# Optimization experiments

Hardware: AMD Instinct MI355X
Metric: run time of the kernel (lower is better)

The kernel has to match this reference:

```python
import jax, jax.numpy as jnp
import numpy as np

HID, H, KV, D = 2048, 16, 4, 128
ROPE_THETA = 10000.0
GATE_NORM = 16.0


def _rope_cos_sin(n, d, dtype=jnp.float32):
    inv_freq = 1.0 / (ROPE_THETA ** (jnp.arange(0, d, 2, dtype=jnp.float32) / d))
    freqs = jnp.arange(n, dtype=jnp.float32)[:, None] * inv_freq[None, :]  # (n, d/2)
    cos = jnp.cos(freqs).astype(dtype)[None, :, None, :]  # (1, n, 1, d/2)
    sin = jnp.sin(freqs).astype(dtype)[None, :, None, :]
    return cos, sin


def _apply_rotary(x, cos, sin):
    # x: (b, n, h, d); rotate-half (NeoX) convention over full head dim
    x1, x2 = jnp.split(x, 2, axis=-1)
    return jnp.concatenate([x1 * cos - x2 * sin, x2 * cos + x1 * sin], axis=-1)


def setup_inputs() -> dict:
    key = jax.random.key(0)
    k1, k2, k3, k4, k5 = jax.random.split(key, 5)
    s = 0.02  # realistic init scale for weights
    return {
        "hidden_states": jax.random.normal(k1, (1, 2048, HID), dtype=jnp.float32),
        "Wq": jax.random.normal(k2, (HID, H * D), dtype=jnp.float32) * s,
        "Wk": jax.random.normal(k3, (HID, KV * D), dtype=jnp.float32) * s,
        "Wv": jax.random.normal(k4, (HID, KV * D), dtype=jnp.float32) * s,
        "Wo": jax.random.normal(k5, (H * D, HID), dtype=jnp.float32) * s,
    }


def _forward(hidden_states, Wq, Wk, Wv, Wo):
    b, n, _ = hidden_states.shape
    groups = H // KV

    q = hidden_states @ Wq            # (b, n, H*D)
    k = hidden_states @ Wk            # (b, n, KV*D)
    v = hidden_states @ Wv            # (b, n, KV*D)
    # pool_g: AdaptiveAvgPool1d(KV*D) on a length-(KV*D) last dim == identity
    g = k

    q = q.reshape(b, n, H, D)
    k = k.reshape(b, n, KV, D)
    v = v.reshape(b, n, KV, D)
    g = g.reshape(b, n, KV, D)

    # GQA repeat to H heads
    k = jnp.repeat(k, groups, axis=2)
    v = jnp.repeat(v, groups, axis=2)
    g = jnp.repeat(g, groups, axis=2)

    sq, sk, sv = q, k, v  # raw (pre-softmax) tensors for the attention branch

    # GLA branch inputs: softmax'd q/k, log-sigmoid gates
    qs = jax.nn.softmax(q.astype(jnp.float32), axis=-1)
    ks = jax.nn.softmax(k.astype(jnp.float32), axis=-1)
    gl = jax.nn.log_sigmoid(g.astype(jnp.float32)) / GATE_NORM

    # rotary on raw q/k (seqlen_offset = 0)
    cos, sin = _rope_cos_sin(n, D)
    sq = _apply_rotary(sq, cos, sin)
    sk = _apply_rotary(sk, cos, sin)

    # --- gated linear attention recurrence (chunk_gla math, scale=1) ---
    def step(S, inp):
        q_t, k_t, v_t, g_t = inp  # each (b, H, D)
        S = S * jnp.exp(g_t)[..., None] + k_t[..., None] * v_t[..., None, :]
        o_t = jnp.einsum('bhk,bhkv->bhv', q_t, S)
        return S, o_t

    xs = tuple(jnp.moveaxis(a, 1, 0) for a in (qs, ks, v, gl))  # (n, b, H, D)
    S0 = jnp.zeros((b, H, D, D), dtype=jnp.float32)
    _, o_gla = jax.lax.scan(step, S0, xs)
    o_gla = jnp.moveaxis(o_gla, 0, 1)  # (b, n, H, D)

    # --- causal softmax attention (flash_attn_func, full window) ---
    scale = D ** -0.5
    scores = jnp.einsum('bqhd,bkhd->bhqk', sq, sk) * scale
    causal = jnp.tril(jnp.ones((n, n), dtype=bool))
    scores = jnp.where(causal[None, None], scores, jnp.finfo(scores.dtype).min)
    attn = jax.nn.softmax(scores, axis=-1)
    y = jnp.einsum('bhqk,bkhd->bqhd', attn, sv)

    o = 0.5 * y + 0.5 * o_gla
    o = o.reshape(b, n, H * D).astype(hidden_states.dtype)
    return o @ Wo


def reference(hidden_states, Wq, Wk, Wv, Wo):
    return _forward(hidden_states, Wq, Wk, Wv, Wo)
```

## Files before the change

### kernel.cpp

```cpp
#include <hip/hip_runtime.h>
#include <hip/hip_bf16.h>

typedef __bf16 bf16x8 __attribute__((ext_vector_type(8)));
typedef float f32x4 __attribute__((ext_vector_type(4)));
typedef float f32x16 __attribute__((ext_vector_type(16)));
typedef unsigned u32x4 __attribute__((ext_vector_type(4)));

#define MFMA16(a,b,c) __builtin_amdgcn_mfma_f32_16x16x32_bf16((a),(b),(c),0,0,0)
#define MFMA32(a,b,c) __builtin_amdgcn_mfma_f32_32x32x16_bf16((a),(b),(c),0,0,0)

__device__ __forceinline__ float bf2f(const __hip_bfloat16 h){ return __bfloat162float(h); }
__device__ __forceinline__ __hip_bfloat16 f2bf(float f){ return __float2bfloat16(f); }
__device__ __forceinline__ __bf16 f2raw(float f){
  return __builtin_bit_cast(__bf16, __builtin_bit_cast(unsigned short, __float2bfloat16(f)));
}

__device__ __forceinline__ unsigned pk2(float a, float b){
  unsigned lo = __builtin_bit_cast(unsigned short, __float2bfloat16(a));
  unsigned hi = __builtin_bit_cast(unsigned short, __float2bfloat16(b));
  return lo | (hi << 16);
}
__device__ __forceinline__ void pl32swap(unsigned &x, unsigned &y){
  asm volatile("v_permlane32_swap_b32 %0, %1" : "+v"(x), "+v"(y));
}
__device__ __forceinline__ void gload16(const void* g, void* l){
  __builtin_amdgcn_global_load_lds((const __attribute__((address_space(1))) unsigned int*)g,
                                   (__attribute__((address_space(3))) unsigned int*)l, 16, 0, 0);
}

__device__ __forceinline__ size_t pk_idx(int grp, int ntile, int t, int d){
  int t32 = t >> 5, ql = t & 31, i = d >> 4, kh = (d >> 3) & 1, j = d & 7;
  return ((size_t)(grp*ntile + t32)*8 + i)*512 + (kh*32 + ql)*8 + j;
}
__device__ __forceinline__ size_t ep_idx(int grp, int t, int d){
  int t16 = t >> 4, lr = t & 15, f = d >> 5, lg = (d >> 3) & 3, j = d & 7;
  return (((size_t)grp*128 + t16)*4 + f)*512 + (lg*16 + lr)*8 + j;
}

__global__ void k_rope_table(float* __restrict__ ct, float* __restrict__ st){
  int e = blockIdx.x*256 + threadIdx.x;
  if (e >= 2048*64) return;
  int t = e >> 6, d = e & 63;
  float inv = expf(-(float)d * 0.14391156831212787f);
  float ang = (float)t * inv;
  ct[e] = cosf(ang);
  st[e] = sinf(ang);
}

__global__ void k_cvt_bf16(const float* __restrict__ in, __hip_bfloat16* __restrict__ out, int n4){
  int i = blockIdx.x*256 + threadIdx.x;
  if (i >= n4) return;
  float4 v = reinterpret_cast<const float4*>(in)[i];
  ushort4 o;
  o.x = __builtin_bit_cast(unsigned short, f2bf(v.x));
  o.y = __builtin_bit_cast(unsigned short, f2bf(v.y));
  o.z = __builtin_bit_cast(unsigned short, f2bf(v.z));
  o.w = __builtin_bit_cast(unsigned short, f2bf(v.w));
  reinterpret_cast<ushort4*>(out)[i] = o;
}

__global__ __launch_bounds__(256) void k_transpose_w(const float* __restrict__ Wq,
                                                     const float* __restrict__ Wk,
                                                     const float* __restrict__ Wv,
                                                     const float* __restrict__ Wo,
                                                     __hip_bfloat16* __restrict__ WqkvT,
                                                     __hip_bfloat16* __restrict__ WoT){
  __shared__ float tile[64][65];
  int id = blockIdx.x;
  const float* in; __hip_bfloat16* out; int C, bx, by;
  if (id < 1024)      { in=Wq; out=WqkvT;                         C=2048; bx=id&31;          by=id>>5; }
  else if (id < 1280) { int i=id-1024; in=Wk; out=WqkvT+(size_t)2048*2048; C=512; bx=i&7;    by=i>>3; }
  else if (id < 1536) { int i=id-1280; in=Wv; out=WqkvT+(size_t)2560*2048; C=512; bx=i&7;    by=i>>3; }
  else                { int i=id-1536; in=Wo; out=WoT;            C=2048; bx=i&31;           by=i>>5; }
  const int R = 2048;
  int ct_ = bx*64, rt = by*64;
  int tx = threadIdx.x & 63, ty = threadIdx.x >> 6;
  #pragma unroll
  for (int i=0;i<16;++i){ int lr = i*4 + ty; tile[lr][tx] = in[(size_t)(rt+lr)*C + ct_+tx]; }
  __syncthreads();
  #pragma unroll
  for (int i=0;i<16;++i){ int lr = i*4 + ty; out[(size_t)(ct_+lr)*R + rt+tx] = f2bf(tile[tx][lr]); }
}

__global__ __launch_bounds__(128) void k_gemm_lds2(const __hip_bfloat16* __restrict__ A,
                                                   const __hip_bfloat16* __restrict__ BT,
                                                   float* __restrict__ C, int M, int N, int K){
  __shared__ __hip_bfloat16 As[128*64];
  __shared__ __hip_bfloat16 Bs[64*64];
  int nwg = gridDim.x;
  int cpx = nwg >> 3;
  int wg  = blockIdx.x;
  int swz = (wg & 7)*cpx + (wg >> 3);
  int nbx = N >> 6;
  int bn = (swz % nbx)*64, bm = (swz / nbx)*128;
  int tid = threadIdx.x, w = tid >> 6, l = tid & 63, lr = l & 15, lg = l >> 4;
  int wr = w*64;
  int srow = tid >> 3;
  int scol = (tid & 7)*8;
  f32x4 z = {0.f,0.f,0.f,0.f};
  f32x4 acc[4][4];
  #pragma unroll
  for (int i=0;i<4;++i){
    #pragma unroll
    for (int j=0;j<4;++j) acc[i][j] = z;
  }
  for (int bk=0; bk<K; bk+=64){
    #pragma unroll
    for (int i=0;i<8;++i)
      gload16(&A[(size_t)(bm + i*16 + srow)*K + bk + scol], &As[i*1024 + tid*8]);
    #pragma unroll
    for (int i=0;i<4;++i)
      gload16(&BT[(size_t)(bn + i*16 + srow)*K + bk + scol], &Bs[i*1024 + tid*8]);
    __syncthreads();
    __builtin_amdgcn_s_setprio(1);
    #pragma unroll
    for (int kk=0; kk<2; ++kk){
      bf16x8 af[4], bfr[4];
      #pragma unroll
      for (int mi=0;mi<4;++mi) af[mi]  = *reinterpret_cast<const bf16x8*>(&As[(wr+mi*16+lr)*64 + kk*32 + lg*8]);
      #pragma unroll
      for (int ni=0;ni<4;++ni) bfr[ni] = *reinterpret_cast<const bf16x8*>(&Bs[(ni*16+lr)*64 + kk*32 + lg*8]);
      #pragma unroll
      for (int mi=0;mi<4;++mi){
        #pragma unroll
        for (int ni=0;ni<4;++ni)
          acc[mi][ni] = MFMA16(af[mi], bfr[ni], acc[mi][ni]);
      }
    }
    __builtin_amdgcn_s_setprio(0);
    __syncthreads();
  }
  #pragma unroll
  for (int mi=0;mi<4;++mi){
    #pragma unroll
    for (int ni=0;ni<4;++ni){
      #pragma unroll
      for (int r=0;r<4;++r)
        C[(size_t)(bm+wr+mi*16+lg*4+r)*N + (bn+ni*16+lr)] = acc[mi][ni][r];
    }
  }
}

__global__ __launch_bounds__(128) void k_gates(const float* __restrict__ qkv,
                                               float* __restrict__ bt_all,
                                               float* __restrict__ eC){
  int c = blockIdx.x, kv = blockIdx.y, k = threadIdx.x;
  float b = 0.f;
  #pragma unroll 8
  for (int t=0;t<64;++t){
    float x = qkv[(size_t)(c*64+t)*3072 + 2048 + kv*128 + k];
    float gl = (fminf(x,0.f) - log1pf(expf(-fabsf(x)))) * 0.09016844005f;
    b += gl;
    bt_all[(size_t)(c*64+t)*512 + kv*128 + k] = b;
  }
  eC[((size_t)kv*32 + c)*128 + k] = exp2f(b);
}

__global__ __launch_bounds__(256) void k_qkpost(const float* __restrict__ qkv, const float* __restrict__ ct,
                                                const float* __restrict__ st, const float* __restrict__ bt_all,
                                                __hip_bfloat16* __restrict__ qpk, __hip_bfloat16* __restrict__ qep,
                                                __hip_bfloat16* __restrict__ kpk, __hip_bfloat16* __restrict__ ke,
                                                __hip_bfloat16* __restrict__ kep){
  int bid = blockIdx.x;
  int i = threadIdx.x & 63;
  if (bid < 8192){
    int g = bid*4 + (threadIdx.x >> 6);
    int t = g >> 4, h = g & 15;
    size_t base = (size_t)t*3072 + h*128;
    float a = qkv[base + i], b = qkv[base + 64 + i];
    float mx = fmaxf(a,b);
    #pragma unroll
    for (int off=1; off<64; off<<=1) mx = fmaxf(mx, __shfl_xor(mx, off));
    float ea = expf(a-mx), eb = expf(b-mx);
    float sm = ea+eb;
    #pragma unroll
    for (int off=1; off<64; off<<=1) sm += __shfl_xor(sm, off);
    float r = 1.0f/sm;
    const float* bp = &bt_all[(size_t)t*512 + (h>>2)*128];
    qep[ep_idx(h, t, i)]    = f2bf(exp2f(bp[i])    * (ea*r));
    qep[ep_idx(h, t, 64+i)] = f2bf(exp2f(bp[64+i]) * (eb*r));
    const float scale = 0.12751745f;
    float co = ct[t*64+i], si = st[t*64+i];
    qpk[pk_idx(h, 64, t, i)]    = f2bf((a*co - b*si)*scale);
    qpk[pk_idx(h, 64, t, 64+i)] = f2bf((b*co + a*si)*scale);
  } else {
    int g = (bid-8192)*4 + (threadIdx.x >> 6);
    int t = g >> 2, kv = g & 3;
    size_t base = (size_t)t*3072 + 2048 + kv*128;
    float a = qkv[base + i], b = qkv[base + 64 + i];
    float mx = fmaxf(a,b);
    #pragma unroll
    for (int off=1; off<64; off<<=1) mx = fmaxf(mx, __shfl_xor(mx, off));
    float ea = expf(a-mx), eb = expf(b-mx);
    float sm = ea+eb;
    #pragma unroll
    for (int off=1; off<64; off<<=1) sm += __shfl_xor(sm, off);
    float r = 1.0f/sm;
    const float* bp = &bt_all[(size_t)t*512 + kv*128];
    float kea = exp2f(-bp[i])    * (ea*r);
    float keb = exp2f(-bp[64+i]) * (eb*r);
    size_t ob = ((size_t)t*4 + kv)*128;
    ke[ob+i]    = f2bf(kea);
    ke[ob+64+i] = f2bf(keb);
    kep[ep_idx(kv, t, i)]    = f2bf(kea);
    kep[ep_idx(kv, t, 64+i)] = f2bf(keb);
    float co = ct[t*64+i], si = st[t*64+i];
    kpk[pk_idx(kv, 64, t, i)]    = f2bf(a*co - b*si);
    kpk[pk_idx(kv, 64, t, 64+i)] = f2bf(b*co + a*si);
  }
}

__global__ __launch_bounds__(256) void k_vprep(const float* __restrict__ qkv,
                                               __hip_bfloat16* __restrict__ vt,
                                               __hip_bfloat16* __restrict__ vpk,
                                               __hip_bfloat16* __restrict__ vpk16){
  __shared__ float lds[64*132];
  int s = blockIdx.x, kv = blockIdx.y;
  int tid = threadIdx.x;
  #pragma unroll
  for (int it=0; it<8; ++it){
    int i = it*256 + tid;
    int t = i >> 5, dc = (i & 31)*4;
    float4 v = *reinterpret_cast<const float4*>(&qkv[(size_t)(s*64+t)*3072 + 2560 + kv*128 + dc]);
    *reinterpret_cast<float4*>(&lds[t*132 + dc]) = v;
  }
  __syncthreads();
  #pragma unroll
  for (int it=0; it<4; ++it){
    int i = it*256 + tid;
    int d = i >> 3, tg = (i & 7)*8;
    bf16x8 o;
    #pragma unroll
    for (int j=0;j<8;++j) o[j] = f2raw(lds[(tg+j)*132 + d]);
    *reinterpret_cast<bf16x8*>(&vt[((size_t)kv*128 + d)*2048 + s*64 + tg]) = o;
  }
  #pragma unroll
  for (int it=0; it<4; ++it){
    int j2 = it*256 + tid;
    int dt = j2 >> 8, kq = (j2 >> 6) & 3, l = j2 & 63;
    int ts = kq*16 + (l>>5)*8, ds = dt*32 + (l&31);
    bf16x8 o;
    #pragma unroll
    for (int j=0;j<8;++j) o[j] = f2raw(lds[(ts+j)*132 + ds]);
    *reinterpret_cast<bf16x8*>(&vpk[((((size_t)kv*32 + s)*4 + dt)*4 + kq)*512 + l*8]) = o;
  }
  #pragma unroll
  for (int it=0; it<4; ++it){
    int j3 = it*256 + tid;
    int oc = j3 >> 7, f2 = (j3 >> 6) & 1, l = j3 & 63;
    int ts = f2*32 + (l>>4)*8, ds = oc*16 + (l&15);
    bf16x8 o;
    #pragma unroll
    for (int j=0;j<8;++j) o[j] = f2raw(lds[(ts+j)*132 + ds]);
    *reinterpret_cast<bf16x8*>(&vpk16[((((size_t)kv*32 + s)*8 + oc)*2 + f2)*512 + l*8]) = o;
  }
}

__global__ __launch_bounds__(256) void k_ckv(const __hip_bfloat16* __restrict__ ke,
                                             const __hip_bfloat16* __restrict__ vt,
                                             float* __restrict__ ckv){
  __shared__ __hip_bfloat16 kt[128*72];
  int c = blockIdx.x, kv = blockIdx.y;
  int tid = threadIdx.x, w = tid>>6, l = tid&63, lr=l&15, lg=l>>4;
  int wr = (w>>1)*64, wc = (w&1)*64;
  #pragma unroll
  for (int r=0;r<4;++r){
    int idx = r*256 + tid;
    int t  = idx >> 4;
    int k0 = (idx & 15)*8;
    bf16x8 v = *reinterpret_cast<const bf16x8*>(&ke[((size_t)(c*64+t)*4 + kv)*128 + k0]);
    #pragma unroll
    for (int j=0;j<8;++j) kt[(k0+j)*72 + t] = __builtin_bit_cast(__hip_bfloat16, (unsigned short)__builtin_bit_cast(unsigned short, v[j]));
  }
  __syncthreads();
  f32x4 z = {0.f,0.f,0.f,0.f};
  f32x4 acc[4][4];
  #pragma unroll
  for (int i=0;i<4;++i){
    #pragma unroll
    for (int j=0;j<4;++j) acc[i][j]=z;
  }
  size_t sb = (size_t)kv*32 + c;
  #pragma unroll
  for (int kf2=0;kf2<2;++kf2){
    bf16x8 af[4], bfr[4];
    #pragma unroll
    for (int mi=0;mi<4;++mi)
      af[mi] = *reinterpret_cast<const bf16x8*>(&kt[(wr+mi*16+lr)*72 + kf2*32 + lg*8]);
    #pragma unroll
    for (int ni=0;ni<4;++ni)
      bfr[ni] = *reinterpret_cast<const bf16x8*>(&vt[((size_t)kv*128 + wc+ni*16+lr)*2048 + c*64 + kf2*32 + lg*8]);
    #pragma unroll
    for (int mi=0;mi<4;++mi){
      #pragma unroll
      for (int ni=0;ni<4;++ni)
        acc[mi][ni] = MFMA16(af[mi], bfr[ni], acc[mi][ni]);
    }
  }
  #pragma unroll
  for (int mi=0;mi<4;++mi){
    #pragma unroll
    for (int ni=0;ni<4;++ni){
      #pragma unroll
      for (int r=0;r<4;++r)
        ckv[(sb*128 + wr+mi*16+lg*4+r)*128 + wc+ni*16+lr] = acc[mi][ni][r];
    }
  }
}

__global__ __launch_bounds__(256) void k_scan(const float* __restrict__ ckv, const float* __restrict__ eC,
                                              __hip_bfloat16* __restrict__ Stp){
  __shared__ float lds[8*128];
  int kv = blockIdx.y, bx = blockIdx.x;
  int tid = threadIdx.x;
  int kloc = tid >> 5;
  int kd  = bx*8 + kloc;
  int vd  = (tid*4) & 127;
  int oc = tid >> 5, lr = (tid >> 1) & 15, jh = (tid & 1)*4;
  int f  = bx >> 2, lg = bx & 3;
  float s0=0.f,s1=0.f,s2=0.f,s3=0.f;
  size_t sb0 = (size_t)kv*32;
  float e = eC[sb0*128 + kd];
  float4 u = reinterpret_cast<const float4*>(&ckv[(sb0*128 + kd)*128 + vd])[0];
  for (int c=0;c<32;++c){
    size_t sb = sb0 + c;
    float e_n = 0.f; float4 u_n = {0.f,0.f,0.f,0.f};
    if (c < 31){
      e_n = eC[(sb+1)*128 + kd];
      u_n = reinterpret_cast<const float4*>(&ckv[((sb+1)*128 + kd)*128 + vd])[0];
    }
    float4 cur = {s0,s1,s2,s3};
    *reinterpret_cast<float4*>(&lds[kloc*128 + vd]) = cur;
    __syncthreads();
    unsigned w0 = pk2(lds[(jh+0)*128 + oc*16+lr], lds[(jh+1)*128 + oc*16+lr]);
    unsigned w1 = pk2(lds[(jh+2)*128 + oc*16+lr], lds[(jh+3)*128 + oc*16+lr]);
    unsigned* dst = reinterpret_cast<unsigned*>(&Stp[((sb*8+oc)*4+f)*512 + (lg*16+lr)*8 + jh]);
    dst[0]=w0; dst[1]=w1;
    __syncthreads();
    s0 = (s0 + u.x)*e; s1 = (s1 + u.y)*e; s2 = (s2 + u.z)*e; s3 = (s3 + u.w)*e;
    e = e_n; u = u_n;
  }
}

__global__ __launch_bounds__(256) void k_attn(const __hip_bfloat16* __restrict__ qpk,
                                              const __hip_bfloat16* __restrict__ kpk,
                                              const __hip_bfloat16* __restrict__ vpk,
                                              float* __restrict__ ocomb){
  __shared__ __hip_bfloat16 OW[4][32][138];
  __shared__ float mW[4][32], lW[4][32];
  int h = blockIdx.y, kvh = h >> 2;
  int tid = threadIdx.x, w = tid >> 6, l = tid & 63;
  int ql = l & 31, kh = l >> 5;

  #pragma unroll 1
  for (int half=0; half<2; ++half){
    int qt = half ? (63 - (int)blockIdx.x) : (int)blockIdx.x;
    int qbase = qt*32;
    int qg = qbase + ql;

    bf16x8 qf[8];
    #pragma unroll
    for (int i=0;i<8;++i)
      qf[i] = *reinterpret_cast<const bf16x8*>(&qpk[((size_t)(h*64 + qt)*8 + i)*512 + l*8]);

    f32x16 zz = {0.f,0.f,0.f,0.f,0.f,0.f,0.f,0.f,0.f,0.f,0.f,0.f,0.f,0.f,0.f,0.f};
    f32x16 of[4];
    #pragma unroll
    for (int dt=0;dt<4;++dt) of[dt] = zz;
    float m = -1e30f, ll = 0.f;

    int nstep = qt/2 + 1;
    for (int s=w; s<nstep; s+=4){
      int kb = s*64;
      bool last = (s == nstep-1);
      f32x16 s0 = zz, s1 = zz;
      #pragma unroll
      for (int i=0;i<8;++i){
        bf16x8 k0 = *reinterpret_cast<const bf16x8*>(&kpk[((size_t)(kvh*64 + 2*s)*8 + i)*512 + l*8]);
        s0 = MFMA32(k0, qf[i], s0);
      }
      #pragma unroll
      for (int i=0;i<8;++i){
        bf16x8 k1 = *reinterpret_cast<const bf16x8*>(&kpk[((size_t)(kvh*64 + 2*s+1)*8 + i)*512 + l*8]);
        s1 = MFMA32(k1, qf[i], s1);
      }
      if (last){
        #pragma unroll
        for (int r=0;r<16;++r){
          int kr = (r&3) + 8*(r>>2) + 4*kh;
          if (kb + kr > qg)      s0[r] = -1e30f;
          if (kb + 32 + kr > qg) s1[r] = -1e30f;
        }
      }
      float pmax = fmaxf(s0[0], s1[0]);
      #pragma unroll
      for (int r=1;r<16;++r) pmax = fmaxf(pmax, fmaxf(s0[r], s1[r]));
      pmax = fmaxf(pmax, __shfl_xor(pmax, 32));
      if (!__all(pmax <= m + 11.54f)){
        float nm = fmaxf(m, pmax);
        float ef = exp2f(m - nm);
        ll *= ef;
        #pragma unroll
        for (int dt=0;dt<4;++dt){
          #pragma unroll
          for (int r=0;r<16;++r) of[dt][r] *= ef;
        }
        m = nm;
      }
      float ps = 0.f;
      #pragma unroll
      for (int r=0;r<16;++r){ s0[r] = exp2f(s0[r]-m); ps += s0[r]; }
      #pragma unroll
      for (int r=0;r<16;++r){ s1[r] = exp2f(s1[r]-m); ps += s1[r]; }
      ps += __shfl_xor(ps, 32);
      ll += ps;
      unsigned pw[4][4];
      {
        unsigned a,b;
        a = pk2(s0[0],s0[1]);   b = pk2(s0[4],s0[5]);   pl32swap(a,b); pw[0][0]=a; pw[0][2]=b;
        a = pk2(s0[2],s0[3]);   b = pk2(s0[6],s0[7]);   pl32swap(a,b); pw[0][1]=a; pw[0][3]=b;
        a = pk2(s0[8],s0[9]);   b = pk2(s0[12],s0[13]); pl32swap(a,b); pw[1][0]=a; pw[1][2]=b;
        a = pk2(s0[10],s0[11]); b = pk2(s0[14],s0[15]); pl32swap(a,b); pw[1][1]=a; pw[1][3]=b;
        a = pk2(s1[0],s1[1]);   b = pk2(s1[4],s1[5]);   pl32swap(a,b); pw[2][0]=a; pw[2][2]=b;
        a = pk2(s1[2],s1[3]);   b = pk2(s1[6],s1[7]);   pl32swap(a,b); pw[2][1]=a; pw[2][3]=b;
        a = pk2(s1[8],s1[9]);   b = pk2(s1[12],s1[13]); pl32swap(a,b); pw[3][0]=a; pw[3][2]=b;
        a = pk2(s1[10],s1[11]); b = pk2(s1[14],s1[15]); pl32swap(a,b); pw[3][1]=a; pw[3][3]=b;
      }
      #pragma unroll
      for (int dt=0; dt<4; ++dt){
        #pragma unroll
        for (int kq=0; kq<4; ++kq){
          bf16x8 vf = *reinterpret_cast<const bf16x8*>(&vpk[((((size_t)kvh*32 + s)*4 + dt)*4 + kq)*512 + l*8]);
          u32x4 pu = {pw[kq][0], pw[kq][1], pw[kq][2], pw[kq][3]};
          bf16x8 pb = __builtin_bit_cast(bf16x8, pu);
          of[dt] = MFMA32(vf, pb, of[dt]);
        }
      }
    }
    if (kh == 0){ mW[w][ql] = m; lW[w][ql] = ll; }
    #pragma unroll
    for (int dt=0; dt<4; ++dt){
      #pragma unroll
      for (int rp=0; rp<4; ++rp){
        unsigned lo = pk2(of[dt][rp*4+0], of[dt][rp*4+1]);
        unsigned hi = pk2(of[dt][rp*4+2], of[dt][rp*4+3]);
        unsigned* dst = reinterpret_cast<unsigned*>(&OW[w][ql][dt*32 + 8*rp + 4*kh]);
        dst[0] = lo; dst[1] = hi;
      }
    }
    __syncthreads();
    int q = tid >> 3, db = (tid & 7)*16;
    float m0=mW[0][q], m1=mW[1][q], m2=mW[2][q], m3=mW[3][q];
    float ms = fmaxf(fmaxf(m0,m1), fmaxf(m2,m3));
    float fac[4] = {exp2f(m0-ms), exp2f(m1-ms), exp2f(m2-ms), exp2f(m3-ms)};
    float lt = fac[0]*lW[0][q] + fac[1]*lW[1][q] + fac[2]*lW[2][q] + fac[3]*lW[3][q];
    float acc[16];
    #pragma unroll
    for (int j=0;j<16;++j) acc[j] = 0.f;
    #pragma unroll
    for (int wv=0; wv<4; ++wv){
      const unsigned* src = reinterpret_cast<const unsigned*>(&OW[wv][q][db]);
      float fx = fac[wv];
      #pragma unroll
      for (int j=0;j<8;++j){
        unsigned u = src[j];
        acc[2*j]   += fx * __builtin_bit_cast(float, u << 16);
        acc[2*j+1] += fx * __builtin_bit_cast(float, u & 0xffff0000u);
      }
    }
    float inv = 0.5f / lt;
    float4 o0 = {acc[0]*inv, acc[1]*inv, acc[2]*inv, acc[3]*inv};
    float4 o1 = {acc[4]*inv, acc[5]*inv, acc[6]*inv, acc[7]*inv};
    float4 o2 = {acc[8]*inv, acc[9]*inv, acc[10]*inv, acc[11]*inv};
    float4 o3 = {acc[12]*inv, acc[13]*inv, acc[14]*inv, acc[15]*inv};
    float4* dst = reinterpret_cast<float4*>(&ocomb[(size_t)(qbase+q)*2048 + h*128 + db]);
    dst[0]=o0; dst[1]=o1; dst[2]=o2; dst[3]=o3;
    __syncthreads();
  }
}

__global__ __launch_bounds__(256) void k_gla_out(const __hip_bfloat16* __restrict__ qep,
                                                 const __hip_bfloat16* __restrict__ kep,
                                                 const __hip_bfloat16* __restrict__ vpk16,
                                                 const __hip_bfloat16* __restrict__ Stp,
                                                 const float* __restrict__ ocomb,
                                                 __hip_bfloat16* __restrict__ obf){
  __shared__ __hip_bfloat16 ldsp[4*16*72];
  int c = blockIdx.x, h = blockIdx.y, kvh = h >> 2;
  int tid = threadIdx.x, w = tid>>6, l = tid&63, lr = l&15, lg = l>>4;
  int t0 = c*64, r0 = w*16;
  __hip_bfloat16* myp = &ldsp[w*16*72];
  bf16x8 qef[4];
  #pragma unroll
  for (int f=0; f<4; ++f)
    qef[f] = *reinterpret_cast<const bf16x8*>(&qep[(((size_t)h*128 + c*4 + w)*4 + f)*512 + l*8]);
  f32x4 z = {0.f,0.f,0.f,0.f};
  f32x4 of[8];
  #pragma unroll
  for (int oc=0;oc<8;++oc) of[oc]=z;
  __builtin_amdgcn_s_setprio(1);
  #pragma unroll
  for (int oc=0; oc<8; ++oc){
    #pragma unroll
    for (int f=0; f<4; ++f){
      bf16x8 sfr = *reinterpret_cast<const bf16x8*>(&Stp[((((size_t)kvh*32 + c)*8 + oc)*4 + f)*512 + l*8]);
      of[oc] = MFMA16(qef[f], sfr, of[oc]);
    }
  }
  f32x4 sacc[4] = {z,z,z,z};
  #pragma unroll
  for (int cb=0; cb<4; ++cb){
    #pragma unroll
    for (int f=0; f<4; ++f){
      bf16x8 kf = *reinterpret_cast<const bf16x8*>(&kep[(((size_t)kvh*128 + c*4 + cb)*4 + f)*512 + l*8]);
      sacc[cb] = MFMA16(qef[f], kf, sacc[cb]);
    }
  }
  __builtin_amdgcn_s_setprio(0);
  #pragma unroll
  for (int cb=0; cb<4; ++cb){
    #pragma unroll
    for (int r=0;r<4;++r){
      int s_ = cb*16 + lr;
      int t_ = r0 + lg*4 + r;
      float v = (s_ <= t_) ? sacc[cb][r] : 0.f;
      myp[(lg*4 + r)*72 + cb*16 + lr] = f2bf(v);
    }
  }
  bf16x8 pf[2];
  #pragma unroll
  for (int kf2=0;kf2<2;++kf2)
    pf[kf2] = *reinterpret_cast<const bf16x8*>(&myp[lr*72 + kf2*32 + lg*8]);
  __builtin_amdgcn_s_setprio(1);
  #pragma unroll
  for (int oc=0; oc<8; ++oc){
    #pragma unroll
    for (int kf2=0;kf2<2;++kf2){
      bf16x8 vf = *reinterpret_cast<const bf16x8*>(&vpk16[((((size_t)kvh*32 + c)*8 + oc)*2 + kf2)*512 + l*8]);
      of[oc] = MFMA16(pf[kf2], vf, of[oc]);
    }
  }
  __builtin_amdgcn_s_setprio(0);
  #pragma unroll
  for (int oc=0;oc<8;++oc){
    #pragma unroll
    for (int r=0;r<4;++r){
      int row = t0 + r0 + lg*4 + r;
      int col = h*128 + oc*16 + lr;
      float prev = ocomb[(size_t)row*2048 + col];
      obf[(size_t)row*2048 + col] = f2bf(prev + 0.5f*of[oc][r]);
    }
  }
}

extern "C" void kernel_launch(void* const* d_in, const int* in_sizes, int n_in,
                              void* d_out, int out_size, void* d_ws, size_t ws_size,
                              hipStream_t stream) {
  const float* hs = (const float*)d_in[0];
  const float* Wq = (const float*)d_in[1];
  const float* Wk = (const float*)d_in[2];
  const float* Wv = (const float*)d_in[3];
  const float* Wo = (const float*)d_in[4];
  float* out = (float*)d_out;

  char* base = (char*)d_ws;
  size_t off = 0;
  auto alloc = [&](size_t bytes) -> void* {
    void* p = base + off;
    off = (off + bytes + 255) & ~(size_t)255;
    return p;
  };

  float*          ropeC  = (float*)alloc(2048*64*4);
  float*          ropeS  = (float*)alloc(2048*64*4);
  __hip_bfloat16* hsb    = (__hip_bfloat16*)alloc((size_t)4194304*2);
  __hip_bfloat16* WqkvT  = (__hip_bfloat16*)alloc((size_t)3072*2048*2);
  __hip_bfloat16* WoT    = (__hip_bfloat16*)alloc((size_t)4194304*2);
  float*          qkv    = (float*)alloc((size_t)2048*3072*4);
  __hip_bfloat16* qpk    = (__hip_bfloat16*)alloc((size_t)4194304*2);
  __hip_bfloat16* kpk    = (__hip_bfloat16*)alloc((size_t)1048576*2);
  __hip_bfloat16* vt     = (__hip_bfloat16*)alloc((size_t)1048576*2);
  __hip_bfloat16* vpk    = (__hip_bfloat16*)alloc((size_t)1048576*2);
  __hip_bfloat16* vpk16  = (__hip_bfloat16*)alloc((size_t)1048576*2);
  __hip_bfloat16* qep    = (__hip_bfloat16*)alloc((size_t)4194304*2);
  __hip_bfloat16* ke     = (__hip_bfloat16*)alloc((size_t)1048576*2);
  __hip_bfloat16* kep    = (__hip_bfloat16*)alloc((size_t)1048576*2);
  float*          bt_all = (float*)alloc((size_t)1048576*4);
  float*          eC     = (float*)alloc((size_t)4*32*128*4);
  float*          ckv    = (float*)alloc((size_t)4*32*128*128*4);
  __hip_bfloat16* Stp    = (__hip_bfloat16*)alloc((size_t)4*32*128*128*2);
  float*          ocomb  = qkv;
  __hip_bfloat16* obf    = hsb;

  if (off > ws_size) return;

  k_rope_table<<<512, 256, 0, stream>>>(ropeC, ropeS);
  k_cvt_bf16<<<4096, 256, 0, stream>>>(hs, hsb, 1048576);
  k_transpose_w<<<dim3(2560), 256, 0, stream>>>(Wq, Wk, Wv, Wo, WqkvT, WoT);

  k_gemm_lds2<<<dim3(768), 128, 0, stream>>>(hsb, WqkvT, qkv, 2048, 3072, 2048);

  k_gates<<<dim3(32,4), 128, 0, stream>>>(qkv, bt_all, eC);
  k_qkpost<<<dim3(10240), 256, 0, stream>>>(qkv, ropeC, ropeS, bt_all, qpk, qep, kpk, ke, kep);
  k_vprep<<<dim3(32,4), 256, 0, stream>>>(qkv, vt, vpk, vpk16);

  k_ckv<<<dim3(32,4), 256, 0, stream>>>(ke, vt, ckv);
  k_scan<<<dim3(16,4), 256, 0, stream>>>(ckv, eC, Stp);

  k_attn<<<dim3(32,16), 256, 0, stream>>>(qpk, kpk, vpk, ocomb);
  k_gla_out<<<dim3(32,16), 256, 0, stream>>>(qep, kep, vpk16, Stp, ocomb, obf);

  k_gemm_lds2<<<dim3(512), 128, 0, stream>>>(obf, WoT, out, 2048, 2048, 2048);
}
```

Baseline: 268.0 us.

## Split attention blocks to one query tile each and halve LDS merge buffer

```diff
diff --git a/kernel.cpp b/kernel.cpp
--- a/kernel.cpp
+++ b/kernel.cpp
@@ -346,136 +346,168 @@
                                               const __hip_bfloat16* __restrict__ kpk,
                                               const __hip_bfloat16* __restrict__ vpk,
                                               float* __restrict__ ocomb){
-  __shared__ __hip_bfloat16 OW[4][32][138];
+  __shared__ __hip_bfloat16 OW[4][32][70];
   __shared__ float mW[4][32], lW[4][32];
   int h = blockIdx.y, kvh = h >> 2;
   int tid = threadIdx.x, w = tid >> 6, l = tid & 63;
   int ql = l & 31, kh = l >> 5;
-
-  #pragma unroll 1
-  for (int half=0; half<2; ++half){
-    int qt = half ? (63 - (int)blockIdx.x) : (int)blockIdx.x;
-    int qbase = qt*32;
-    int qg = qbase + ql;
-
-    bf16x8 qf[8];
-    #pragma unroll
-    for (int i=0;i<8;++i)
-      qf[i] = *reinterpret_cast<const bf16x8*>(&qpk[((size_t)(h*64 + qt)*8 + i)*512 + l*8]);
-
-    f32x16 zz = {0.f,0.f,0.f,0.f,0.f,0.f,0.f,0.f,0.f,0.f,0.f,0.f,0.f,0.f,0.f,0.f};
-    f32x16 of[4];
-    #pragma unroll
-    for (int dt=0;dt<4;++dt) of[dt] = zz;
-    float m = -1e30f, ll = 0.f;
-
-    int nstep = qt/2 + 1;
-    for (int s=w; s<nstep; s+=4){
-      int kb = s*64;
-      bool last = (s == nstep-1);
-      f32x16 s0 = zz, s1 = zz;
-      #pragma unroll
-      for (int i=0;i<8;++i){
-        bf16x8 k0 = *reinterpret_cast<const bf16x8*>(&kpk[((size_t)(kvh*64 + 2*s)*8 + i)*512 + l*8]);
-        s0 = MFMA32(k0, qf[i], s0);
+  int qt = 63 - (int)blockIdx.x;
+  int qbase = qt*32;
+  int qg = qbase + ql;
+
+  bf16x8 qf[8];
+  #pragma unroll
+  for (int i=0;i<8;++i)
+    qf[i] = *reinterpret_cast<const bf16x8*>(&qpk[((size_t)(h*64 + qt)*8 + i)*512 + l*8]);
+
+  f32x16 zz = {0.f,0.f,0.f,0.f,0.f,0.f,0.f,0.f,0.f,0.f,0.f,0.f,0.f,0.f,0.f,0.f};
+  f32x16 of[4];
+  #pragma unroll
+  for (int dt=0;dt<4;++dt) of[dt] = zz;
+  float m = -1e30f, ll = 0.f;
+
+  int nstep = qt/2 + 1;
+  for (int s=w; s<nstep; s+=4){
+    int kb = s*64;
+    bool last = (s == nstep-1);
+    f32x16 s0 = zz, s1 = zz;
+    #pragma unroll
+    for (int i=0;i<8;++i){
+      bf16x8 k0 = *reinterpret_cast<const bf16x8*>(&kpk[((size_t)(kvh*64 + 2*s)*8 + i)*512 + l*8]);
+      s0 = MFMA32(k0, qf[i], s0);
+    }
+    #pragma unroll
+    for (int i=0;i<8;++i){
+      bf16x8 k1 = *reinterpret_cast<const bf16x8*>(&kpk[((size_t)(kvh*64 + 2*s+1)*8 + i)*512 + l*8]);
+      s1 = MFMA32(k1, qf[i], s1);
+    }
+    if (last){
+      #pragma unroll
+      for (int r=0;r<16;++r){
+        int kr = (r&3) + 8*(r>>2) + 4*kh;
+        if (kb + kr > qg)      s0[r] = -1e30f;
+        if (kb + 32 + kr > qg) s1[r] = -1e30f;
       }
-      #pragma unroll
-      for (int i=0;i<8;++i){
-        bf16x8 k1 = *reinterpret_cast<const bf16x8*>(&kpk[((size_t)(kvh*64 + 2*s+1)*8 + i)*512 + l*8]);
-        s1 = MFMA32(k1, qf[i], s1);
+    }
+    float pmax = fmaxf(s0[0], s1[0]);
+    #pragma unroll
+    for (int r=1;r<16;++r) pmax = fmaxf(pmax, fmaxf(s0[r], s1[r]));
+    pmax = fmaxf(pmax, __shfl_xor(pmax, 32));
+    if (!__all(pmax <= m + 11.54f)){
+      float nm = fmaxf(m, pmax);
+      float ef = exp2f(m - nm);
+      ll *= ef;
+      #pragma unroll
+      for (int dt=0;dt<4;++dt){
+        #pragma unroll
+        for (int r=0;r<16;++r) of[dt][r] *= ef;
       }
-      if (last){
-        #pragma unroll
-        for (int r=0;r<16;++r){
-          int kr = (r&3) + 8*(r>>2) + 4*kh;
-          if (kb + kr > qg)      s0[r] = -1e30f;
-          if (kb + 32 + kr > qg) s1[r] = -1e30f;
-        }
+      m = nm;
+    }
+    float ps = 0.f;
+    #pragma unroll
+    for (int r=0;r<16;++r){ s0[r] = exp2f(s0[r]-m); ps += s0[r]; }
+    #pragma unroll
+    for (int r=0;r<16;++r){ s1[r] = exp2f(s1[r]-m); ps += s1[r]; }
+    ps += __shfl_xor(ps, 32);
+    ll += ps;
+    unsigned pw[4][4];
+    {
+      unsigned a,b;
+      a = pk2(s0[0],s0[1]);   b = pk2(s0[4],s0[5]);   pl32swap(a,b); pw[0][0]=a; pw[0][2]=b;
+      a = pk2(s0[2],s0[3]);   b = pk2(s0[6],s0[7]);   pl32swap(a,b); pw[0][1]=a; pw[0][3]=b;
+      a = pk2(s0[8],s0[9]);   b = pk2(s0[12],s0[13]); pl32swap(a,b); pw[1][0]=a; pw[1][2]=b;
+      a = pk2(s0[10],s0[11]); b = pk2(s0[14],s0[15]); pl32swap(a,b); pw[1][1]=a; pw[1][3]=b;
+      a = pk2(s1[0],s1[1]);   b = pk2(s1[4],s1[5]);   pl32swap(a,b); pw[2][0]=a; pw[2][2]=b;
+      a = pk2(s1[2],s1[3]);   b = pk2(s1[6],s1[7]);   pl32swap(a,b); pw[2][1]=a; pw[2][3]=b;
+      a = pk2(s1[8],s1[9]);   b = pk2(s1[12],s1[13]); pl32swap(a,b); pw[3][0]=a; pw[3][2]=b;
+      a = pk2(s1[10],s1[11]); b = pk2(s1[14],s1[15]); pl32swap(a,b); pw[3][1]=a; pw[3][3]=b;
+    }
+    #pragma unroll
+    for (int dt=0; dt<4; ++dt){
+      #pragma unroll
+      for (int kq=0; kq<4; ++kq){
+        bf16x8 vf = *reinterpret_cast<const bf16x8*>(&vpk[((((size_t)kvh*32 + s)*4 + dt)*4 + kq)*512 + l*8]);
+        u32x4 pu = {pw[kq][0], pw[kq][1], pw[kq][2], pw[kq][3]};
+        bf16x8 pb = __builtin_bit_cast(bf16x8, pu);
+        of[dt] = MFMA32(vf, pb, of[dt]);
       }
-      float pmax = fmaxf(s0[0], s1[0]);
-      #pragma unroll
-      for (int r=1;r<16;++r) pmax = fmaxf(pmax, fmaxf(s0[r], s1[r]));
-      pmax = fmaxf(pmax, __shfl_xor(pmax, 32));
-      if (!__all(pmax <= m + 11.54f)){
-        float nm = fmaxf(m, pmax);
-        float ef = exp2f(m - nm);
-        ll *= ef;
-        #pragma unroll
-        for (int dt=0;dt<4;++dt){
-          #pragma unroll
-          for (int r=0;r<16;++r) of[dt][r] *= ef;
-        }
-        m = nm;
-      }
-      float ps = 0.f;
-      #pragma unroll
-      for (int r=0;r<16;++r){ s0[r] = exp2f(s0[r]-m); ps += s0[r]; }
-      #pragma unroll
-      for (int r=0;r<16;++r){ s1[r] = exp2f(s1[r]-m); ps += s1[r]; }
-      ps += __shfl_xor(ps, 32);
-      ll += ps;
-      unsigned pw[4][4];
-      {
-        unsigned a,b;
-        a = pk2(s0[0],s0[1]);   b = pk2(s0[4],s0[5]);   pl32swap(a,b); pw[0][0]=a; pw[0][2]=b;
-        a = pk2(s0[2],s0[3]);   b = pk2(s0[6],s0[7]);   pl32swap(a,b); pw[0][1]=a; pw[0][3]=b;
-        a = pk2(s0[8],s0[9]);   b = pk2(s0[12],s0[13]); pl32swap(a,b); pw[1][0]=a; pw[1][2]=b;
-        a = pk2(s0[10],s0[11]); b = pk2(s0[14],s0[15]); pl32swap(a,b); pw[1][1]=a; pw[1][3]=b;
-        a = pk2(s1[0],s1[1]);   b = pk2(s1[4],s1[5]);   pl32swap(a,b); pw[2][0]=a; pw[2][2]=b;
-        a = pk2(s1[2],s1[3]);   b = pk2(s1[6],s1[7]);   pl32swap(a,b); pw[2][1]=a; pw[2][3]=b;
-        a = pk2(s1[8],s1[9]);   b = pk2(s1[12],s1[13]); pl32swap(a,b); pw[3][0]=a; pw[3][2]=b;
-        a = pk2(s1[10],s1[11]); b = pk2(s1[14],s1[15]); pl32swap(a,b); pw[3][1]=a; pw[3][3]=b;
-      }
-      #pragma unroll
-      for (int dt=0; dt<4; ++dt){
-        #pragma unroll
-        for (int kq=0; kq<4; ++kq){
-          bf16x8 vf = *reinterpret_cast<const bf16x8*>(&vpk[((((size_t)kvh*32 + s)*4 + dt)*4 + kq)*512 + l*8]);
-          u32x4 pu = {pw[kq][0], pw[kq][1], pw[kq][2], pw[kq][3]};
-          bf16x8 pb = __builtin_bit_cast(bf16x8, pu);
-          of[dt] = MFMA32(vf, pb, of[dt]);
-        }
-      }
-    }
-    if (kh == 0){ mW[w][ql] = m; lW[w][ql] = ll; }
-    #pragma unroll
-    for (int dt=0; dt<4; ++dt){
-      #pragma unroll
-      for (int rp=0; rp<4; ++rp){
-        unsigned lo = pk2(of[dt][rp*4+0], of[dt][rp*4+1]);
-        unsigned hi = pk2(of[dt][rp*4+2], of[dt][rp*4+3]);
-        unsigned* dst = reinterpret_cast<unsigned*>(&OW[w][ql][dt*32 + 8*rp + 4*kh]);
-        dst[0] = lo; dst[1] = hi;
-      }
-    }
-    __syncthreads();
-    int q = tid >> 3, db = (tid & 7)*16;
+    }
+  }
+  if (kh == 0){ mW[w][ql] = m; lW[w][ql] = ll; }
+  int q = tid >> 3, db8 = (tid & 7)*8;
+  float fac0, fac1, fac2, fac3, lt;
+  #pragma unroll
+  for (int dt=0; dt<2; ++dt){
+    #pragma unroll
+    for (int rp=0; rp<4; ++rp){
+      unsigned lo = pk2(of[dt][rp*4+0], of[dt][rp*4+1]);
+      unsigned hi = pk2(of[dt][rp*4+2], of[dt][rp*4+3]);
+      unsigned* dst = reinterpret_cast<unsigned*>(&OW[w][ql][dt*32 + 8*rp + 4*kh]);
+      dst[0] = lo; dst[1] = hi;
+    }
+  }
+  __syncthreads();
+  {
     float m0=mW[0][q], m1=mW[1][q], m2=mW[2][q], m3=mW[3][q];
     float ms = fmaxf(fmaxf(m0,m1), fmaxf(m2,m3));
-    float fac[4] = {exp2f(m0-ms), exp2f(m1-ms), exp2f(m2-ms), exp2f(m3-ms)};
-    float lt = fac[0]*lW[0][q] + fac[1]*lW[1][q] + fac[2]*lW[2][q] + fac[3]*lW[3][q];
-    float acc[16];
-    #pragma unroll
-    for (int j=0;j<16;++j) acc[j] = 0.f;
+    fac0=exp2f(m0-ms); fac1=exp2f(m1-ms); fac2=exp2f(m2-ms); fac3=exp2f(m3-ms);
+    lt = fac0*lW[0][q] + fac1*lW[1][q] + fac2*lW[2][q] + fac3*lW[3][q];
+  }
+  float inv = 0.5f / lt;
+  {
+    float acc[8];
+    #pragma unroll
+    for (int j=0;j<8;++j) acc[j] = 0.f;
+    float facv[4] = {fac0, fac1, fac2, fac3};
     #pragma unroll
     for (int wv=0; wv<4; ++wv){
-      const unsigned* src = reinterpret_cast<const unsigned*>(&OW[wv][q][db]);
-      float fx = fac[wv];
-      #pragma unroll
-      for (int j=0;j<8;++j){
+      const unsigned* src = reinterpret_cast<const unsigned*>(&OW[wv][q][db8]);
+      float fx = facv[wv];
+      #pragma unroll
+      for (int j=0;j<4;++j){
         unsigned u = src[j];
         acc[2*j]   += fx * __builtin_bit_cast(float, u << 16);
         acc[2*j+1] += fx * __builtin_bit_cast(float, u & 0xffff0000u);
       }
     }
-    float inv = 0.5f / lt;
     float4 o0 = {acc[0]*inv, acc[1]*inv, acc[2]*inv, acc[3]*inv};
     float4 o1 = {acc[4]*inv, acc[5]*inv, acc[6]*inv, acc[7]*inv};
-    float4 o2 = {acc[8]*inv, acc[9]*inv, acc[10]*inv, acc[11]*inv};
-    float4 o3 = {acc[12]*inv, acc[13]*inv, acc[14]*inv, acc[15]*inv};
-    float4* dst = reinterpret_cast<float4*>(&ocomb[(size_t)(qbase+q)*2048 + h*128 + db]);
-    dst[0]=o0; dst[1]=o1; dst[2]=o2; dst[3]=o3;
-    __syncthreads();
+    float4* dst = reinterpret_cast<float4*>(&ocomb[(size_t)(qbase+q)*2048 + h*128 + db8]);
+    dst[0]=o0; dst[1]=o1;
+  }
+  __syncthreads();
+  #pragma unroll
+  for (int dt=0; dt<2; ++dt){
+    #pragma unroll
+    for (int rp=0; rp<4; ++rp){
+      unsigned lo = pk2(of[dt+2][rp*4+0], of[dt+2][rp*4+1]);
+      unsigned hi = pk2(of[dt+2][rp*4+2], of[dt+2][rp*4+3]);
+      unsigned* dst = reinterpret_cast<unsigned*>(&OW[w][ql][dt*32 + 8*rp + 4*kh]);
+      dst[0] = lo; dst[1] = hi;
+    }
+  }
+  __syncthreads();
+  {
+    float acc[8];
+    #pragma unroll
+    for (int j=0;j<8;++j) acc[j] = 0.f;
+    float facv[4] = {fac0, fac1, fac2, fac3};
+    #pragma unroll
+    for (int wv=0; wv<4; ++wv){
+      const unsigned* src = reinterpret_cast<const unsigned*>(&OW[wv][q][db8]);
+      float fx = facv[wv];
+      #pragma unroll
+      for (int j=0;j<4;++j){
+        unsigned u = src[j];
+        acc[2*j]   += fx * __builtin_bit_cast(float, u << 16);
+        acc[2*j+1] += fx * __builtin_bit_cast(float, u & 0xffff0000u);
+      }
+    }
+    float4 o0 = {acc[0]*inv, acc[1]*inv, acc[2]*inv, acc[3]*inv};
+    float4 o1 = {acc[4]*inv, acc[5]*inv, acc[6]*inv, acc[7]*inv};
+    float4* dst = reinterpret_cast<float4*>(&ocomb[(size_t)(qbase+q)*2048 + h*128 + 64 + db8]);
+    dst[0]=o0; dst[1]=o1;
   }
 }
 
@@ -607,7 +639,7 @@
   k_ckv<<<dim3(32,4), 256, 0, stream>>>(ke, vt, ckv);
   k_scan<<<dim3(16,4), 256, 0, stream>>>(ckv, eC, Stp);
 
-  k_attn<<<dim3(32,16), 256, 0, stream>>>(qpk, kpk, vpk, ocomb);
+  k_attn<<<dim3(64,16), 256, 0, stream>>>(qpk, kpk, vpk, ocomb);
   k_gla_out<<<dim3(32,16), 256, 0, stream>>>(qep, kep, vpk16, Stp, ocomb, obf);
 
   k_gemm_lds2<<<dim3(512), 128, 0, stream>>>(obf, WoT, out, 2048, 2048, 2048);
```

Result: no change. 268.9 us (+0.4%).
